# Optimization experiments

Hardware: AMD Instinct MI355X
Metric: run time of the kernel (lower is better)

The kernel has to match this reference:

```python
import jax, jax.numpy as jnp
import numpy as np

ENC_LEN, B, ENC2, DEC, E = 1024, 64, 1024, 512, 512

def setup_inputs() -> dict:
    key = jax.random.key(0)
    k1, k2, k3, k4 = jax.random.split(key, 4)
    enc_output = jax.random.normal(k1, (ENC_LEN, B, ENC2), dtype=jnp.float32)
    s = jax.random.normal(k2, (1, B, DEC), dtype=jnp.float32)
    # torch Linear weights: [out_features, in_features], no bias
    W_attn = jax.random.normal(k3, (E, ENC2 + DEC), dtype=jnp.float32) * (1.0 / np.sqrt(ENC2 + DEC))
    W_v = jax.random.normal(k4, (1, E), dtype=jnp.float32) * (1.0 / np.sqrt(E))
    return {"enc_output": enc_output, "s": s, "W_attn": W_attn, "W_v": W_v}

def reference(enc_output, s, W_attn, W_v):
    # cat([enc_output, s.repeat(L,1,1)], -1) @ W_attn.T  ==  enc @ Wa_e.T + s @ Wa_s.T (broadcast)
    enc2 = enc_output.shape[-1]
    Wa_e = W_attn[:, :enc2]          # [E, 2*enc_hid]
    Wa_s = W_attn[:, enc2:]          # [E, dec_hid]
    pre = jnp.einsum('lbc,ec->lbe', enc_output, Wa_e) + jnp.einsum('obd,ed->obe', s, Wa_s)
    engry = jnp.tanh(pre)            # [L, B, E]
    attention = jnp.einsum('lbe,oe->lbo', engry, W_v)[..., 0].T  # [B, L]
    return jax.nn.softmax(attention, axis=-1)
```

## Files before the change

kernel.cpp:

```cpp
#include <hip/hip_runtime.h>
#include <hip/hip_bf16.h>
#include <stdint.h>

typedef __bf16 bf16;
typedef __bf16 bf16x4 __attribute__((ext_vector_type(4)));
typedef __bf16 bf16x8 __attribute__((ext_vector_type(8)));
typedef float  f32x4  __attribute__((ext_vector_type(4)));

#define L_TOT 1024
#define B_TOT 64
#define C_TOT 1024
#define D_TOT 512
#define E_TOT 512
#define M_TOT (L_TOT * B_TOT)
#define K_TOT C_TOT
#define W_LD  (C_TOT + D_TOT)

#define BM 128
#define BN 512
#define BK 64
#define NTHREADS 512
#define NKT (K_TOT / BK)

__device__ __forceinline__ void gload_lds16(const void* g, void* l) {
  __builtin_amdgcn_global_load_lds(
      (const __attribute__((address_space(1))) unsigned int*)(uintptr_t)g,
      (__attribute__((address_space(3))) unsigned int*)(uintptr_t)l,
      16, 0, 0);
}

__device__ __forceinline__ bf16x4 cvt4(float4 v) {
  bf16x4 o;
  o[0] = (bf16)v.x; o[1] = (bf16)v.y; o[2] = (bf16)v.z; o[3] = (bf16)v.w;
  return o;
}

__global__ void convert_we_kernel(const float* __restrict__ Wattn,
                                  bf16* __restrict__ Wb) {
  const int e = blockIdx.x;
  const int t = threadIdx.x;
  const float4 v = ((const float4*)(Wattn + (size_t)e * W_LD))[t];
  ((bf16x4*)(Wb + (size_t)e * C_TOT))[t] = cvt4(v);
}

__global__ void sb_kernel(const float* __restrict__ s,
                          const float* __restrict__ Wattn,
                          float* __restrict__ sb) {
  const int e = blockIdx.x;
  const int b = threadIdx.x;
  const float4* sr = (const float4*)(s + (size_t)b * D_TOT);
  const float4* wr = (const float4*)(Wattn + (size_t)e * W_LD + C_TOT);
  float acc = 0.f;
#pragma unroll 4
  for (int i = 0; i < D_TOT / 4; ++i) {
    float4 a = sr[i], w = wr[i];
    acc += a.x * w.x; acc += a.y * w.y; acc += a.z * w.z; acc += a.w * w.w;
  }
  sb[(size_t)b * E_TOT + e] = acc;
}

__global__ __launch_bounds__(NTHREADS, 2)
void gemm_tanh_dot_kernel(const float* __restrict__ A,
                          const bf16*  __restrict__ Wb,
                          const float* __restrict__ sb,
                          const float* __restrict__ Wv,
                          float* __restrict__ logits) {
  __shared__ __align__(16) char smem[(BM * BK + BN * BK) * 2];
  char* As = smem;
  char* Bs = smem + BM * BK * 2;

  const int tid  = threadIdx.x;
  const int lane = tid & 63;
  const int wid  = tid >> 6;
  const int wm   = wid >> 2;
  const int wn   = wid & 3;
  const int fr   = lane & 15;
  const int fg   = lane >> 4;
  const int m0   = blockIdx.x * BM;

  const int a_row = tid >> 4;
  const int a_col = tid & 15;
  const float* aG = A + (size_t)(m0 + a_row) * K_TOT + a_col * 4;
  const int a_sw  = ((((a_col >> 1) ^ (a_row & 7)) << 4) | ((a_col & 1) << 3));

  const int b_row = (wid << 6) + (lane >> 3);
  const int b_xor = ((lane & 7) ^ (lane >> 3)) << 3;
  const bf16* bG  = Wb + (size_t)b_row * K_TOT + b_xor;
  char* b_dst     = Bs + (wid << 13) + (lane << 4);

  f32x4 acc[4][8];
#pragma unroll
  for (int i = 0; i < 4; ++i)
#pragma unroll
    for (int j = 0; j < 8; ++j)
      acc[i][j] = (f32x4){0.f, 0.f, 0.f, 0.f};

  const char* Arow = As + ((wm << 6) + fr) * 128;
  const char* Brow = Bs + ((wn << 7) + fr) * 128;

  float4 av0 = *(const float4*)(aG);
  float4 av1 = *(const float4*)(aG + 32 * K_TOT);
  float4 av2 = *(const float4*)(aG + 64 * K_TOT);
  float4 av3 = *(const float4*)(aG + 96 * K_TOT);

#pragma unroll 1
  for (int kt = 0; kt < NKT; ++kt) {
    const int k0 = kt * BK;
    __syncthreads();
#pragma unroll
    for (int i = 0; i < 8; ++i)
      gload_lds16(bG + k0 + i * 8 * K_TOT, b_dst + i * 1024);
    *(bf16x4*)(As + (a_row +  0) * 128 + a_sw) = cvt4(av0);
    *(bf16x4*)(As + (a_row + 32) * 128 + a_sw) = cvt4(av1);
    *(bf16x4*)(As + (a_row + 64) * 128 + a_sw) = cvt4(av2);
    *(bf16x4*)(As + (a_row + 96) * 128 + a_sw) = cvt4(av3);
    __syncthreads();
    const int k1 = (kt + 1 < NKT) ? (k0 + BK) : 0;
    av0 = *(const float4*)(aG + k1);
    av1 = *(const float4*)(aG + k1 + 32 * K_TOT);
    av2 = *(const float4*)(aG + k1 + 64 * K_TOT);
    av3 = *(const float4*)(aG + k1 + 96 * K_TOT);
#pragma unroll
    for (int kk = 0; kk < 2; ++kk) {
      const int xo = (((kk << 2) + fg) ^ (fr & 7)) << 4;
      bf16x8 af[4];
      bf16x8 bfrag[8];
#pragma unroll
      for (int am = 0; am < 4; ++am)
        af[am] = *(const bf16x8*)(Arow + (am << 4) * 128 + xo);
#pragma unroll
      for (int bn = 0; bn < 8; ++bn)
        bfrag[bn] = *(const bf16x8*)(Brow + (bn << 4) * 128 + xo);
#pragma unroll
      for (int am = 0; am < 4; ++am)
#pragma unroll
        for (int bn = 0; bn < 8; ++bn)
          acc[am][bn] = __builtin_amdgcn_mfma_f32_16x16x32_bf16(
              af[am], bfrag[bn], acc[am][bn], 0, 0, 0);
    }
  }

  float wv[8];
#pragma unroll
  for (int bn = 0; bn < 8; ++bn)
    wv[bn] = Wv[(wn << 7) + (bn << 4) + fr];

  float sums[4][4];
#pragma unroll
  for (int am = 0; am < 4; ++am) {
#pragma unroll
    for (int j = 0; j < 4; ++j) {
      const int mloc = (wm << 6) + (am << 4) + (fg << 2) + j;
      const int b = (m0 + mloc) & 63;
      const float* sbr = sb + (size_t)b * E_TOT + (wn << 7) + fr;
      float c = 0.f;
#pragma unroll
      for (int bn = 0; bn < 8; ++bn) {
        float v = acc[am][bn][j] + sbr[bn << 4];
        c += tanhf(v) * wv[bn];
      }
      c += __shfl_xor(c, 1, 64);
      c += __shfl_xor(c, 2, 64);
      c += __shfl_xor(c, 4, 64);
      c += __shfl_xor(c, 8, 64);
      sums[am][j] = c;
    }
  }

  __syncthreads();
  float* red = (float*)smem;
  if (fr == 0) {
#pragma unroll
    for (int am = 0; am < 4; ++am)
#pragma unroll
      for (int j = 0; j < 4; ++j)
        red[(wn << 7) + (wm << 6) + (am << 4) + (fg << 2) + j] = sums[am][j];
  }
  __syncthreads();
  if (tid < BM) {
    float v = red[tid] + red[128 + tid] + red[256 + tid] + red[384 + tid];
    logits[m0 + tid] = v;
  }
}

__global__ __launch_bounds__(256)
void softmax_kernel(const float* __restrict__ logits, float* __restrict__ out) {
  const int b = blockIdx.x;
  const int t = threadIdx.x;
  const int lane = t & 63, w = t >> 6;
  __shared__ float sm[8];
  float x[4];
  float mx = -3.4e38f;
#pragma unroll
  for (int i = 0; i < 4; ++i) {
    const int l = t + (i << 8);
    x[i] = logits[(size_t)l * 64 + b];
    mx = fmaxf(mx, x[i]);
  }
#pragma unroll
  for (int off = 1; off < 64; off <<= 1)
    mx = fmaxf(mx, __shfl_xor(mx, off, 64));
  if (lane == 0) sm[w] = mx;
  __syncthreads();
  mx = fmaxf(fmaxf(sm[0], sm[1]), fmaxf(sm[2], sm[3]));
  float ex[4], ssum = 0.f;
#pragma unroll
  for (int i = 0; i < 4; ++i) { ex[i] = expf(x[i] - mx); ssum += ex[i]; }
#pragma unroll
  for (int off = 1; off < 64; off <<= 1)
    ssum += __shfl_xor(ssum, off, 64);
  if (lane == 0) sm[4 + w] = ssum;
  __syncthreads();
  const float inv = 1.0f / (sm[4] + sm[5] + sm[6] + sm[7]);
#pragma unroll
  for (int i = 0; i < 4; ++i)
    out[(size_t)b * 1024 + t + (i << 8)] = ex[i] * inv;
}

extern "C" void kernel_launch(void* const* d_in, const int* in_sizes, int n_in,
                              void* d_out, int out_size, void* d_ws, size_t ws_size,
                              hipStream_t stream) {
  const float* enc = (const float*)d_in[0];
  const float* s   = (const float*)d_in[1];
  const float* Wat = (const float*)d_in[2];
  const float* Wv  = (const float*)d_in[3];
  float* out = (float*)d_out;

  char* ws = (char*)d_ws;
  bf16*  Wb     = (bf16*)ws;
  float* sb     = (float*)(ws + (1u << 20));
  float* logits = (float*)(ws + (1u << 20) + (128u << 10));

  convert_we_kernel<<<E_TOT, 256, 0, stream>>>(Wat, Wb);
  sb_kernel<<<E_TOT, 64, 0, stream>>>(s, Wat, sb);
  gemm_tanh_dot_kernel<<<M_TOT / BM, NTHREADS, 0, stream>>>(enc, Wb, sb, Wv, logits);
  softmax_kernel<<<B_TOT, 256, 0, stream>>>(logits, out);
}
```

Baseline: 183.4 us.

## Double-buffer LDS tiles with smaller BM/BK and one sync per k-step

Restructures the fused GEMM-tanh-dot kernel to use double-buffered LDS for A and B, so the next k-tile is staged while MFMAs run on the current one. Only one barrier is needed per iteration. Block tile shrinks to 64 rows and BK=32, with 8 waves each covering 64 output columns and a new swizzle layout. The smaller tile and larger launch bound target higher occupancy, at the cost of more B-tile reloads per row of A (lower reuse of W) and a heavier final cross-wave reduction.

New measurement: 178.6 us. -2.6%, faster.

```diff
diff --git a/kernel.cpp b/kernel.cpp
--- a/kernel.cpp
+++ b/kernel.cpp
@@ -13,14 +13,13 @@
 #define D_TOT 512
 #define E_TOT 512
 #define M_TOT (L_TOT * B_TOT)
-#define K_TOT C_TOT
 #define W_LD  (C_TOT + D_TOT)
 
-#define BM 128
+#define BM 64
 #define BN 512
-#define BK 64
-#define NTHREADS 512
-#define NKT (K_TOT / BK)
+#define BK 32
+#define NT 512
+#define NKT (C_TOT / BK)
 
 __device__ __forceinline__ void gload_lds16(const void* g, void* l) {
   __builtin_amdgcn_global_load_lds(
@@ -59,126 +58,114 @@
   sb[(size_t)b * E_TOT + e] = acc;
 }
 
-__global__ __launch_bounds__(NTHREADS, 2)
+__global__ __launch_bounds__(NT, 4)
 void gemm_tanh_dot_kernel(const float* __restrict__ A,
                           const bf16*  __restrict__ Wb,
                           const float* __restrict__ sb,
                           const float* __restrict__ Wv,
                           float* __restrict__ logits) {
-  __shared__ __align__(16) char smem[(BM * BK + BN * BK) * 2];
-  char* As = smem;
-  char* Bs = smem + BM * BK * 2;
+  __shared__ __align__(16) char smem[2 * 4096 + 2 * 32768];
+  char* const As0 = smem;
+  char* const As1 = smem + 4096;
+  char* const Bs0 = smem + 8192;
+  char* const Bs1 = smem + 8192 + 32768;
 
   const int tid  = threadIdx.x;
   const int lane = tid & 63;
-  const int wid  = tid >> 6;
-  const int wm   = wid >> 2;
-  const int wn   = wid & 3;
+  const int wn   = tid >> 6;
   const int fr   = lane & 15;
   const int fg   = lane >> 4;
   const int m0   = blockIdx.x * BM;
 
-  const int a_row = tid >> 4;
-  const int a_col = tid & 15;
-  const float* aG = A + (size_t)(m0 + a_row) * K_TOT + a_col * 4;
-  const int a_sw  = ((((a_col >> 1) ^ (a_row & 7)) << 4) | ((a_col & 1) << 3));
-
-  const int b_row = (wid << 6) + (lane >> 3);
-  const int b_xor = ((lane & 7) ^ (lane >> 3)) << 3;
-  const bf16* bG  = Wb + (size_t)b_row * K_TOT + b_xor;
-  char* b_dst     = Bs + (wid << 13) + (lane << 4);
-
-  f32x4 acc[4][8];
+  const int a_row = tid >> 3;
+  const int a_k4  = (tid & 7) << 2;
+  const float* gA = A + (size_t)(m0 + a_row) * C_TOT + a_k4;
+  const int a_s   = ((a_row & 1) << 2) | (a_k4 >> 3);
+  const int aw_off = ((a_row >> 1) << 7)
+                   + ((a_s ^ ((a_row >> 1) & 7)) << 4)
+                   + ((a_k4 & 4) << 1);
+
+  const int b_s = (tid & 7) ^ ((tid >> 3) & 7);
+  const int b_e = ((tid >> 3) << 1) + (b_s >> 2);
+  const bf16* bsrc = Wb + (size_t)b_e * C_TOT + ((b_s & 3) << 3);
+  const int b_dst = tid << 4;
+
+  const int xo = ((((fr & 1) << 2) | fg) ^ ((fr >> 1) & 7)) << 4;
+  const int ro = ((fr >> 1) << 7) + xo;
+
+  f32x4 acc[4][4];
 #pragma unroll
   for (int i = 0; i < 4; ++i)
 #pragma unroll
-    for (int j = 0; j < 8; ++j)
+    for (int j = 0; j < 4; ++j)
       acc[i][j] = (f32x4){0.f, 0.f, 0.f, 0.f};
 
-  const char* Arow = As + ((wm << 6) + fr) * 128;
-  const char* Brow = Bs + ((wn << 7) + fr) * 128;
-
-  float4 av0 = *(const float4*)(aG);
-  float4 av1 = *(const float4*)(aG + 32 * K_TOT);
-  float4 av2 = *(const float4*)(aG + 64 * K_TOT);
-  float4 av3 = *(const float4*)(aG + 96 * K_TOT);
-
+  float4 avA = *(const float4*)(gA);
+#pragma unroll
+  for (int i = 0; i < 4; ++i)
+    gload_lds16(bsrc + i * 131072, Bs0 + b_dst + i * 8192);
+  *(bf16x4*)(As0 + aw_off) = cvt4(avA);
+  avA = *(const float4*)(gA + BK);
+  __syncthreads();
+
+  char* Ac = As0; char* An = As1; char* Bc = Bs0; char* Bn = Bs1;
 #pragma unroll 1
   for (int kt = 0; kt < NKT; ++kt) {
-    const int k0 = kt * BK;
+    if (kt + 1 < NKT) {
+      const int k1 = (kt + 1) * BK;
+#pragma unroll
+      for (int i = 0; i < 4; ++i)
+        gload_lds16(bsrc + k1 + i * 131072, Bn + b_dst + i * 8192);
+      *(bf16x4*)(An + aw_off) = cvt4(avA);
+      const int k2 = (kt + 2 < NKT) ? (kt + 2) * BK : 0;
+      avA = *(const float4*)(gA + k2);
+    }
+    bf16x8 af[4], bfr[4];
+#pragma unroll
+    for (int am = 0; am < 4; ++am)
+      af[am] = *(const bf16x8*)(Ac + am * 1024 + ro);
+#pragma unroll
+    for (int bn = 0; bn < 4; ++bn)
+      bfr[bn] = *(const bf16x8*)(Bc + (wn << 12) + bn * 1024 + ro);
+#pragma unroll
+    for (int am = 0; am < 4; ++am)
+#pragma unroll
+      for (int bn = 0; bn < 4; ++bn)
+        acc[am][bn] = __builtin_amdgcn_mfma_f32_16x16x32_bf16(
+            af[am], bfr[bn], acc[am][bn], 0, 0, 0);
     __syncthreads();
-#pragma unroll
-    for (int i = 0; i < 8; ++i)
-      gload_lds16(bG + k0 + i * 8 * K_TOT, b_dst + i * 1024);
-    *(bf16x4*)(As + (a_row +  0) * 128 + a_sw) = cvt4(av0);
-    *(bf16x4*)(As + (a_row + 32) * 128 + a_sw) = cvt4(av1);
-    *(bf16x4*)(As + (a_row + 64) * 128 + a_sw) = cvt4(av2);
-    *(bf16x4*)(As + (a_row + 96) * 128 + a_sw) = cvt4(av3);
-    __syncthreads();
-    const int k1 = (kt + 1 < NKT) ? (k0 + BK) : 0;
-    av0 = *(const float4*)(aG + k1);
-    av1 = *(const float4*)(aG + k1 + 32 * K_TOT);
-    av2 = *(const float4*)(aG + k1 + 64 * K_TOT);
-    av3 = *(const float4*)(aG + k1 + 96 * K_TOT);
-#pragma unroll
-    for (int kk = 0; kk < 2; ++kk) {
-      const int xo = (((kk << 2) + fg) ^ (fr & 7)) << 4;
-      bf16x8 af[4];
-      bf16x8 bfrag[8];
-#pragma unroll
-      for (int am = 0; am < 4; ++am)
-        af[am] = *(const bf16x8*)(Arow + (am << 4) * 128 + xo);
-#pragma unroll
-      for (int bn = 0; bn < 8; ++bn)
-        bfrag[bn] = *(const bf16x8*)(Brow + (bn << 4) * 128 + xo);
-#pragma unroll
-      for (int am = 0; am < 4; ++am)
-#pragma unroll
-        for (int bn = 0; bn < 8; ++bn)
-          acc[am][bn] = __builtin_amdgcn_mfma_f32_16x16x32_bf16(
-              af[am], bfrag[bn], acc[am][bn], 0, 0, 0);
-    }
-  }
-
-  float wv[8];
-#pragma unroll
-  for (int bn = 0; bn < 8; ++bn)
-    wv[bn] = Wv[(wn << 7) + (bn << 4) + fr];
-
-  float sums[4][4];
+    char* t0 = Ac; Ac = An; An = t0;
+    char* t1 = Bc; Bc = Bn; Bn = t1;
+  }
+
+  float wv[4];
+#pragma unroll
+  for (int bn = 0; bn < 4; ++bn)
+    wv[bn] = Wv[(wn << 6) + (bn << 4) + fr];
+
+  float* red = (float*)smem;
 #pragma unroll
   for (int am = 0; am < 4; ++am) {
 #pragma unroll
     for (int j = 0; j < 4; ++j) {
-      const int mloc = (wm << 6) + (am << 4) + (fg << 2) + j;
-      const int b = (m0 + mloc) & 63;
-      const float* sbr = sb + (size_t)b * E_TOT + (wn << 7) + fr;
+      const int mloc = (am << 4) + (fg << 2) + j;
+      const float* sbr = sb + (size_t)mloc * E_TOT + (wn << 6) + fr;
       float c = 0.f;
 #pragma unroll
-      for (int bn = 0; bn < 8; ++bn) {
-        float v = acc[am][bn][j] + sbr[bn << 4];
-        c += tanhf(v) * wv[bn];
-      }
+      for (int bn = 0; bn < 4; ++bn)
+        c += tanhf(acc[am][bn][j] + sbr[bn << 4]) * wv[bn];
       c += __shfl_xor(c, 1, 64);
       c += __shfl_xor(c, 2, 64);
       c += __shfl_xor(c, 4, 64);
       c += __shfl_xor(c, 8, 64);
-      sums[am][j] = c;
+      if (fr == 0) red[(wn << 6) + mloc] = c;
     }
   }
-
-  __syncthreads();
-  float* red = (float*)smem;
-  if (fr == 0) {
-#pragma unroll
-    for (int am = 0; am < 4; ++am)
-#pragma unroll
-      for (int j = 0; j < 4; ++j)
-        red[(wn << 7) + (wm << 6) + (am << 4) + (fg << 2) + j] = sums[am][j];
-  }
   __syncthreads();
   if (tid < BM) {
-    float v = red[tid] + red[128 + tid] + red[256 + tid] + red[384 + tid];
+    float v = 0.f;
+#pragma unroll
+    for (int w = 0; w < 8; ++w) v += red[(w << 6) + tid];
     logits[m0 + tid] = v;
   }
 }
@@ -233,6 +220,6 @@
 
   convert_we_kernel<<<E_TOT, 256, 0, stream>>>(Wat, Wb);
   sb_kernel<<<E_TOT, 64, 0, stream>>>(s, Wat, sb);
-  gemm_tanh_dot_kernel<<<M_TOT / BM, NTHREADS, 0, stream>>>(enc, Wb, sb, Wv, logits);
+  gemm_tanh_dot_kernel<<<M_TOT / BM, NT, 0, stream>>>(enc, Wb, sb, Wv, logits);
   softmax_kernel<<<B_TOT, 256, 0, stream>>>(logits, out);
 }
```
